# Kernel optimization log

Measured on AMD Instinct MI355X. Metric: run time of the kernel, lower is better.

## Reference

```python
import jax, jax.numpy as jnp
import numpy as np

N_NODES = 50000
N_EDGES = 800000
IN_FEATS = 128
H_FEATS = 128
NUM_CLASSES = 2


def setup_inputs() -> dict:
    key = jax.random.key(0)
    ks = jax.random.split(key, 6)
    in_feat = jax.random.normal(ks[0], (N_NODES, IN_FEATS), dtype=jnp.float32)
    src = jax.random.randint(ks[1], (N_EDGES,), 0, N_NODES, dtype=jnp.int64)
    dst = jax.random.randint(ks[2], (N_EDGES,), 0, N_NODES, dtype=jnp.int64)
    W_self = jax.random.normal(ks[3], (H_FEATS, IN_FEATS), dtype=jnp.float32) / np.sqrt(IN_FEATS)
    W_neigh = jax.random.normal(ks[4], (H_FEATS, IN_FEATS), dtype=jnp.float32) / np.sqrt(IN_FEATS)
    b_neigh = jnp.zeros((H_FEATS,), dtype=jnp.float32)
    W_fc = jax.random.normal(ks[5], (NUM_CLASSES, H_FEATS), dtype=jnp.float32) / np.sqrt(H_FEATS)
    b_fc = jnp.zeros((NUM_CLASSES,), dtype=jnp.float32)
    return {"in_feat": in_feat, "src": src, "dst": dst, "W_self": W_self,
            "W_neigh": W_neigh, "b_neigh": b_neigh, "W_fc": W_fc, "b_fc": b_fc}


def reference(in_feat, src, dst, W_self, W_neigh, b_neigh, W_fc, b_fc):
    # SAGEConv mean aggregation: mean of src features over incoming edges per dst
    gathered = in_feat[src]                                        # [E, F_in]
    summed = jax.ops.segment_sum(gathered, dst, num_segments=N_NODES)  # [N, F_in]
    deg = jax.ops.segment_sum(jnp.ones((src.shape[0],), in_feat.dtype), dst,
                              num_segments=N_NODES)                # [N]
    h_neigh = summed / jnp.maximum(deg, 1.0)[:, None]
    # h = fc_self(x) + fc_neigh(h_neigh) + bias
    h = in_feat @ W_self.T + h_neigh @ W_neigh.T + b_neigh
    h = jax.nn.relu(h)
    logits = h @ W_fc.T + b_fc
    return jax.nn.sigmoid(logits)
```

## Files before the change

kernel.cpp:

```cpp
#include <hip/hip_runtime.h>
#include <hip/hip_fp8.h>
#include <math.h>

#define N_NODES 50000
#define N_EDGES 800000
#define FEATS 128
#define KTOT 256
#define NCLASS 2
#define NSB 196
#define NXCD 8
#define DRANGE 6250
#define SC_CHUNKS 384
#define GM_BPR 1563

typedef __attribute__((ext_vector_type(8))) short bf16x8;
typedef __attribute__((ext_vector_type(4))) float f32x4;

__device__ __forceinline__ float bflo(unsigned u) {
    return __uint_as_float(u << 16);
}
__device__ __forceinline__ float bfhi(unsigned u) {
    return __uint_as_float(u & 0xffff0000u);
}
__device__ __forceinline__ unsigned f2bf(float f) {
    unsigned u = __float_as_uint(f);
    return (u + 0x7fffu + ((u >> 16) & 1u)) >> 16;
}
__device__ __forceinline__ unsigned char f2q(float f) {
    __hip_fp8_e4m3 t(f);
    return (unsigned char)t.__x;
}
__device__ __forceinline__ float q2f(unsigned b) {
    __hip_fp8_e4m3 t;
    t.__x = (__hip_fp8_storage_t)(b & 0xffu);
    return (float)t;
}

#define CASTX_BLOCKS 3125
#define CASTW_BLOCKS 64

__global__ __launch_bounds__(256) void cast_prep(
    const float* __restrict__ x,
    const float* __restrict__ Ws, const float* __restrict__ Wn,
    unsigned short* __restrict__ xh, unsigned char* __restrict__ xq,
    unsigned short* __restrict__ wcat)
{
    int b = blockIdx.x;
    if (b < CASTX_BLOCKS) {
        size_t i = ((size_t)b * 256 + threadIdx.x) * 8;
        float4 v0 = *(const float4*)(x + i);
        float4 v1 = *(const float4*)(x + i + 4);
        uint4 o;
        o.x = f2bf(v0.x) | (f2bf(v0.y) << 16);
        o.y = f2bf(v0.z) | (f2bf(v0.w) << 16);
        o.z = f2bf(v1.x) | (f2bf(v1.y) << 16);
        o.w = f2bf(v1.z) | (f2bf(v1.w) << 16);
        *(uint4*)(xh + i) = o;
        uint2 q;
        q.x = (unsigned)f2q(v0.x) | ((unsigned)f2q(v0.y) << 8) |
              ((unsigned)f2q(v0.z) << 16) | ((unsigned)f2q(v0.w) << 24);
        q.y = (unsigned)f2q(v1.x) | ((unsigned)f2q(v1.y) << 8) |
              ((unsigned)f2q(v1.z) << 16) | ((unsigned)f2q(v1.w) << 24);
        *(uint2*)(xq + i) = q;
    } else {
        int i = (b - CASTX_BLOCKS) * 512 + threadIdx.x * 2;
        int n = i >> 8, k = i & 255;
        float a0 = (k < 128) ? Ws[n * 128 + k] : Wn[n * 128 + k - 128];
        float a1 = (k + 1 < 128) ? Ws[n * 128 + k + 1] : Wn[n * 128 + k + 1 - 128];
        *(unsigned*)(wcat + i) = f2bf(a0) | (f2bf(a1) << 16);
    }
}

__global__ __launch_bounds__(256) void hist_local(
    const int* __restrict__ dst, int* __restrict__ degi)
{
    const int r = blockIdx.x & (NXCD - 1);
    const int c = blockIdx.x >> 3;
    const int lo = r * DRANGE;
    const int hi = lo + DRANGE;
    const int CH = (N_EDGES + SC_CHUNKS - 1) / SC_CHUNKS;
    const int ebeg = c * CH;
    const int eend = (ebeg + CH < N_EDGES) ? ebeg + CH : N_EDGES;

    for (int e = ebeg + threadIdx.x; e < eend; e += 256) {
        int d = dst[e];
        if (d >= lo && d < hi) atomicAdd(&degi[d], 1);
    }
}

__global__ __launch_bounds__(256) void scan1(
    const int* __restrict__ degi, int* __restrict__ incl, int* __restrict__ bsum)
{
    __shared__ int sh[256];
    const int t = threadIdx.x;
    const int i = blockIdx.x * 256 + t;
    int d = (i < N_NODES) ? degi[i] : 0;
    sh[t] = d;
    __syncthreads();
#pragma unroll
    for (int off = 1; off < 256; off <<= 1) {
        int v = sh[t];
        int u = (t >= off) ? sh[t - off] : 0;
        __syncthreads();
        sh[t] = v + u;
        __syncthreads();
    }
    int iv = sh[t];
    if (i < N_NODES) incl[i] = iv;
    if (t == 255) bsum[blockIdx.x] = iv;
}

__global__ __launch_bounds__(256) void scan2(
    const int* __restrict__ degi, const int* __restrict__ incl,
    const int* __restrict__ bsum, int* __restrict__ offs, int* __restrict__ cursor)
{
    __shared__ int sh[256];
    const int t = threadIdx.x;
    const int b = blockIdx.x;
    sh[t] = (t < b) ? bsum[t] : 0;
    __syncthreads();
#pragma unroll
    for (int off = 128; off > 0; off >>= 1) {
        if (t < off) sh[t] += sh[t + off];
        __syncthreads();
    }
    const int bo = sh[0];
    const int i = b * 256 + t;
    if (i < N_NODES) {
        int o = bo + incl[i] - degi[i];
        offs[i] = o;
        cursor[i] = o;
    }
    if (b == 0 && t == 0) offs[N_NODES] = N_EDGES;
}

__global__ __launch_bounds__(256) void scatter_idx(
    const int* __restrict__ src, const int* __restrict__ dst,
    int* __restrict__ cursor, int* __restrict__ eidx)
{
    const int r = blockIdx.x & (NXCD - 1);
    const int c = blockIdx.x >> 3;
    const int lo = r * DRANGE;
    const int hi = lo + DRANGE;
    const int CH = (N_EDGES + SC_CHUNKS - 1) / SC_CHUNKS;
    const int ebeg = c * CH;
    const int eend = (ebeg + CH < N_EDGES) ? ebeg + CH : N_EDGES;

    for (int e = ebeg + threadIdx.x; e < eend; e += 256) {
        int d = dst[e];
        if (d >= lo && d < hi) {
            int pos = atomicAdd(&cursor[d], 1);
            eidx[pos] = src[e];
        }
    }
}

__global__ __launch_bounds__(256) void gather_mean(
    const uint2* __restrict__ xq2, const int* __restrict__ eidx,
    const int* __restrict__ offs, uint4* __restrict__ hh4)
{
    const int r = blockIdx.x & (NXCD - 1);
    const int nir = (blockIdx.x >> 3) * 4 + (threadIdx.x >> 6);
    if (nir >= DRANGE) return;
    const int node = r * DRANGE + nir;
    const int l = threadIdx.x & 63;
    const int q = l >> 4, j = l & 15;
    const int beg = offs[node];
    const int end = offs[node + 1];

    float acc[8] = {0, 0, 0, 0, 0, 0, 0, 0};
    int e = beg + q;
    for (; e + 12 < end; e += 16) {
#pragma unroll
        for (int u = 0; u < 4; u++) {
            int row = eidx[e + u * 4];
            uint2 v = xq2[(size_t)row * 16 + j];
            acc[0] += q2f(v.x);       acc[1] += q2f(v.x >> 8);
            acc[2] += q2f(v.x >> 16); acc[3] += q2f(v.x >> 24);
            acc[4] += q2f(v.y);       acc[5] += q2f(v.y >> 8);
            acc[6] += q2f(v.y >> 16); acc[7] += q2f(v.y >> 24);
        }
    }
    for (; e < end; e += 4) {
        int row = eidx[e];
        uint2 v = xq2[(size_t)row * 16 + j];
        acc[0] += q2f(v.x);       acc[1] += q2f(v.x >> 8);
        acc[2] += q2f(v.x >> 16); acc[3] += q2f(v.x >> 24);
        acc[4] += q2f(v.y);       acc[5] += q2f(v.y >> 8);
        acc[6] += q2f(v.y >> 16); acc[7] += q2f(v.y >> 24);
    }

#pragma unroll
    for (int off = 16; off < 64; off <<= 1) {
#pragma unroll
        for (int i = 0; i < 8; i++) acc[i] += __shfl_xor(acc[i], off);
    }

    if (q == 0) {
        const float rd = 1.0f / fmaxf((float)(end - beg), 1.0f);
        uint4 o;
        o.x = f2bf(acc[0] * rd) | (f2bf(acc[1] * rd) << 16);
        o.y = f2bf(acc[2] * rd) | (f2bf(acc[3] * rd) << 16);
        o.z = f2bf(acc[4] * rd) | (f2bf(acc[5] * rd) << 16);
        o.w = f2bf(acc[6] * rd) | (f2bf(acc[7] * rd) << 16);
        hh4[(size_t)node * 16 + j] = o;
    }
}

__global__ __launch_bounds__(256) void node_mfma(
    const unsigned short* __restrict__ xh, const unsigned short* __restrict__ hh,
    const unsigned short* __restrict__ wcat,
    const float* __restrict__ bn, const float* __restrict__ wfc,
    const float* __restrict__ bfc, float* __restrict__ out)
{
    const int wid = threadIdx.x >> 6;
    const int l = threadIdx.x & 63;
    const int node0 = blockIdx.x * 128 + wid * 32;
    const int fr = l & 15, fq = l >> 4;

    float bnv[8], w0v[8], w1v[8];
#pragma unroll
    for (int nt = 0; nt < 8; nt++) {
        int f = nt * 16 + fr;
        bnv[nt] = bn[f];
        w0v[nt] = wfc[f];
        w1v[nt] = wfc[FEATS + f];
    }

    f32x4 acc[2][8] = {};

#pragma unroll
    for (int ks = 0; ks < 8; ks++) {
        const unsigned short* abase = (ks < 4) ? xh : hh;
        const int ka = (ks & 3) * 32 + fq * 8;
        const int kb = ks * 32 + fq * 8;

        bf16x8 bfr[8];
#pragma unroll
        for (int nt = 0; nt < 8; nt++) {
            int n = nt * 16 + fr;
            bfr[nt] = *(const bf16x8*)(wcat + (size_t)n * KTOT + kb);
        }
#pragma unroll
        for (int rt = 0; rt < 2; rt++) {
            int row = node0 + rt * 16 + fr;
            row = (row < N_NODES) ? row : N_NODES - 1;
            bf16x8 afr = *(const bf16x8*)(abase + (size_t)row * FEATS + ka);
#pragma unroll
            for (int nt = 0; nt < 8; nt++)
                acc[rt][nt] = __builtin_amdgcn_mfma_f32_16x16x32_bf16(
                    afr, bfr[nt], acc[rt][nt], 0, 0, 0);
        }
    }

    const float b0 = bfc[0], b1 = bfc[1];
#pragma unroll
    for (int rt = 0; rt < 2; rt++) {
        float p0[4] = {0, 0, 0, 0}, p1[4] = {0, 0, 0, 0};
#pragma unroll
        for (int nt = 0; nt < 8; nt++) {
#pragma unroll
            for (int r = 0; r < 4; r++) {
                float h = fmaxf(acc[rt][nt][r] + bnv[nt], 0.f);
                p0[r] += h * w0v[nt];
                p1[r] += h * w1v[nt];
            }
        }
#pragma unroll
        for (int off = 1; off < 16; off <<= 1) {
#pragma unroll
            for (int r = 0; r < 4; r++) {
                p0[r] += __shfl_xor(p0[r], off);
                p1[r] += __shfl_xor(p1[r], off);
            }
        }
        if (fr == 0) {
#pragma unroll
            for (int r = 0; r < 4; r++) {
                int node = node0 + rt * 16 + fq * 4 + r;
                if (node < N_NODES) {
                    float2 o;
                    o.x = 1.f / (1.f + expf(-(p0[r] + b0)));
                    o.y = 1.f / (1.f + expf(-(p1[r] + b1)));
                    *(float2*)(out + (size_t)node * NCLASS) = o;
                }
            }
        }
    }
}

extern "C" void kernel_launch(void* const* d_in, const int* in_sizes, int n_in,
                              void* d_out, int out_size, void* d_ws, size_t ws_size,
                              hipStream_t stream) {
    const float* in_feat = (const float*)d_in[0];
    const int*   src     = (const int*)d_in[1];
    const int*   dst     = (const int*)d_in[2];
    const float* Wself   = (const float*)d_in[3];
    const float* Wneigh  = (const float*)d_in[4];
    const float* bneigh  = (const float*)d_in[5];
    const float* Wfc     = (const float*)d_in[6];
    const float* bfc     = (const float*)d_in[7];
    float* out = (float*)d_out;

    int* degi   = (int*)d_ws;
    int* offs   = degi + N_NODES;
    int* cursor = offs + N_NODES + 1;
    int* eidx   = cursor + N_NODES;
    int* incl   = eidx + N_EDGES;
    int* bsum   = incl + N_NODES;
    size_t int_elems = (size_t)N_NODES * 4 + 1 + N_EDGES + 256;
    int_elems = (int_elems + 3) & ~(size_t)3;
    unsigned short* xh   = (unsigned short*)((int*)d_ws + int_elems);
    unsigned short* wcat = xh + (size_t)N_NODES * FEATS;
    unsigned short* hh   = wcat + (size_t)FEATS * KTOT;
    unsigned char*  xq   = (unsigned char*)(hh + (size_t)N_NODES * FEATS);

    hipMemsetAsync(d_ws, 0, (size_t)N_NODES * sizeof(int), stream);

    cast_prep<<<CASTX_BLOCKS + CASTW_BLOCKS, 256, 0, stream>>>(
        in_feat, Wself, Wneigh, xh, xq, wcat);
    hist_local<<<NXCD * SC_CHUNKS, 256, 0, stream>>>(dst, degi);

    scan1<<<NSB, 256, 0, stream>>>(degi, incl, bsum);
    scan2<<<NSB, 256, 0, stream>>>(degi, incl, bsum, offs, cursor);

    scatter_idx<<<NXCD * SC_CHUNKS, 256, 0, stream>>>(src, dst, cursor, eidx);

    gather_mean<<<NXCD * GM_BPR, 256, 0, stream>>>(
        (const uint2*)xq, eidx, offs, (uint4*)hh);

    int nb = (N_NODES + 127) / 128;
    node_mfma<<<nb, 256, 0, stream>>>(xh, hh, wcat, bneigh, Wfc, bfc, out);
}
```

Measured before the change: 219.8 us.

## Pre-bucket edges by destination range to avoid redundant full edge scans

```diff
diff --git a/kernel.cpp b/kernel.cpp
--- a/kernel.cpp
+++ b/kernel.cpp
@@ -10,8 +10,10 @@
 #define NSB 196
 #define NXCD 8
 #define DRANGE 6250
-#define SC_CHUNKS 384
 #define GM_BPR 1563
+#define BP_BLOCKS 1024
+#define BP_CHUNK 782
+#define HB_BPR 64
 
 typedef __attribute__((ext_vector_type(8))) short bf16x8;
 typedef __attribute__((ext_vector_type(4))) float f32x4;
@@ -71,21 +73,45 @@
     }
 }
 
-__global__ __launch_bounds__(256) void hist_local(
-    const int* __restrict__ dst, int* __restrict__ degi)
+__global__ __launch_bounds__(256) void bucket_part(
+    const int* __restrict__ src, const int* __restrict__ dst,
+    int* __restrict__ gcnt,
+    unsigned* __restrict__ bucket)
+{
+    __shared__ int cnt[8], base[8], cur[8];
+    const int b = blockIdx.x, t = threadIdx.x;
+    const int lo = b * BP_CHUNK;
+    const int hi = (lo + BP_CHUNK < N_EDGES) ? lo + BP_CHUNK : N_EDGES;
+    if (t < 8) cnt[t] = 0;
+    __syncthreads();
+    for (int e = lo + t; e < hi; e += 256)
+        atomicAdd(&cnt[dst[e] / DRANGE], 1);
+    __syncthreads();
+    if (t < 8) {
+        base[t] = atomicAdd(&gcnt[t * 16], cnt[t]);
+        cur[t] = 0;
+    }
+    __syncthreads();
+    for (int e = lo + t; e < hi; e += 256) {
+        int d = dst[e], s = src[e];
+        int r = d / DRANGE;
+        int ofs = atomicAdd(&cur[r], 1);
+        bucket[(size_t)r * N_EDGES + base[r] + ofs] =
+            ((unsigned)(d - r * DRANGE) << 16) | (unsigned)s;
+    }
+}
+
+__global__ __launch_bounds__(256) void hist_bucket(
+    const unsigned* __restrict__ bucket, const int* __restrict__ gcnt,
+    int* __restrict__ degi)
 {
     const int r = blockIdx.x & (NXCD - 1);
-    const int c = blockIdx.x >> 3;
+    const int k = blockIdx.x >> 3;
+    const int n = gcnt[r * 16];
+    const unsigned* bk = bucket + (size_t)r * N_EDGES;
     const int lo = r * DRANGE;
-    const int hi = lo + DRANGE;
-    const int CH = (N_EDGES + SC_CHUNKS - 1) / SC_CHUNKS;
-    const int ebeg = c * CH;
-    const int eend = (ebeg + CH < N_EDGES) ? ebeg + CH : N_EDGES;
-
-    for (int e = ebeg + threadIdx.x; e < eend; e += 256) {
-        int d = dst[e];
-        if (d >= lo && d < hi) atomicAdd(&degi[d], 1);
-    }
+    for (int i = k * 256 + threadIdx.x; i < n; i += HB_BPR * 256)
+        atomicAdd(&degi[lo + (int)(bk[i] >> 16)], 1);
 }
 
 __global__ __launch_bounds__(256) void scan1(
@@ -134,24 +160,19 @@
     if (b == 0 && t == 0) offs[N_NODES] = N_EDGES;
 }
 
-__global__ __launch_bounds__(256) void scatter_idx(
-    const int* __restrict__ src, const int* __restrict__ dst,
+__global__ __launch_bounds__(256) void place_bucket(
+    const unsigned* __restrict__ bucket, const int* __restrict__ gcnt,
     int* __restrict__ cursor, int* __restrict__ eidx)
 {
     const int r = blockIdx.x & (NXCD - 1);
-    const int c = blockIdx.x >> 3;
+    const int k = blockIdx.x >> 3;
+    const int n = gcnt[r * 16];
+    const unsigned* bk = bucket + (size_t)r * N_EDGES;
     const int lo = r * DRANGE;
-    const int hi = lo + DRANGE;
-    const int CH = (N_EDGES + SC_CHUNKS - 1) / SC_CHUNKS;
-    const int ebeg = c * CH;
-    const int eend = (ebeg + CH < N_EDGES) ? ebeg + CH : N_EDGES;
-
-    for (int e = ebeg + threadIdx.x; e < eend; e += 256) {
-        int d = dst[e];
-        if (d >= lo && d < hi) {
-            int pos = atomicAdd(&cursor[d], 1);
-            eidx[pos] = src[e];
-        }
+    for (int i = k * 256 + threadIdx.x; i < n; i += HB_BPR * 256) {
+        unsigned p = bk[i];
+        int pos = atomicAdd(&cursor[lo + (int)(p >> 16)], 1);
+        eidx[pos] = (int)(p & 0xFFFFu);
     }
 }
 
@@ -303,28 +324,33 @@
     float* out = (float*)d_out;
 
     int* degi   = (int*)d_ws;
-    int* offs   = degi + N_NODES;
+    int* gcnt   = degi + N_NODES;
+    int* offs   = gcnt + 128;
     int* cursor = offs + N_NODES + 1;
     int* eidx   = cursor + N_NODES;
     int* incl   = eidx + N_EDGES;
     int* bsum   = incl + N_NODES;
-    size_t int_elems = (size_t)N_NODES * 4 + 1 + N_EDGES + 256;
+    unsigned* bucket = (unsigned*)(bsum + 256);
+    size_t int_elems = (size_t)N_NODES * 4 + 128 + 1 + N_EDGES + 256
+                     + (size_t)NXCD * N_EDGES;
     int_elems = (int_elems + 3) & ~(size_t)3;
     unsigned short* xh   = (unsigned short*)((int*)d_ws + int_elems);
     unsigned short* wcat = xh + (size_t)N_NODES * FEATS;
     unsigned short* hh   = wcat + (size_t)FEATS * KTOT;
     unsigned char*  xq   = (unsigned char*)(hh + (size_t)N_NODES * FEATS);
 
-    hipMemsetAsync(d_ws, 0, (size_t)N_NODES * sizeof(int), stream);
+    hipMemsetAsync(d_ws, 0, (size_t)(N_NODES + 128) * sizeof(int), stream);
 
     cast_prep<<<CASTX_BLOCKS + CASTW_BLOCKS, 256, 0, stream>>>(
         in_feat, Wself, Wneigh, xh, xq, wcat);
-    hist_local<<<NXCD * SC_CHUNKS, 256, 0, stream>>>(dst, degi);
+
+    bucket_part<<<BP_BLOCKS, 256, 0, stream>>>(src, dst, gcnt, bucket);
+    hist_bucket<<<NXCD * HB_BPR, 256, 0, stream>>>(bucket, gcnt, degi);
 
     scan1<<<NSB, 256, 0, stream>>>(degi, incl, bsum);
     scan2<<<NSB, 256, 0, stream>>>(degi, incl, bsum, offs, cursor);
 
-    scatter_idx<<<NXCD * SC_CHUNKS, 256, 0, stream>>>(src, dst, cursor, eidx);
+    place_bucket<<<NXCD * HB_BPR, 256, 0, stream>>>(bucket, gcnt, cursor, eidx);
 
     gather_mean<<<NXCD * GM_BPR, 256, 0, stream>>>(
         (const uint2*)xq, eidx, offs, (uint4*)hh);
```

Result: slower. 237.0 us (+7.8%).
